# Performance work log

Hardware: AMD Instinct MI355X
Metric: run time of the kernel (lower is better)

The kernel has to match this reference:

```python
import jax, jax.numpy as jnp
import numpy as np

E, H = 1024, 16
N, S, T = 2, 2048, 2048


def setup_inputs() -> dict:
    key = jax.random.key(0)
    ks = jax.random.split(key, 8)
    scale = 1.0 / np.sqrt(E)
    q = jax.random.normal(ks[0], (N, S, E), dtype=jnp.float32)
    k = jax.random.normal(ks[1], (N, T, E), dtype=jnp.float32)
    v = jax.random.normal(ks[2], (N, T, E), dtype=jnp.float32)
    pad_mask = jax.random.randint(ks[3], (N, 1, 1, T), 0, 2, dtype=jnp.int32)
    subsq_mask = jnp.tril(jnp.ones((S, T), dtype=jnp.int32))[None, None]
    Wq = jax.random.normal(ks[4], (E, E), dtype=jnp.float32) * scale
    Wk = jax.random.normal(ks[5], (E, E), dtype=jnp.float32) * scale
    Wv = jax.random.normal(ks[6], (E, E), dtype=jnp.float32) * scale
    bq = jnp.zeros((E,), dtype=jnp.float32)
    bk = jnp.zeros((E,), dtype=jnp.float32)
    bv = jnp.zeros((E,), dtype=jnp.float32)
    return {"query": q, "key": k, "value": v, "pad_mask": pad_mask,
            "subsq_mask": subsq_mask, "Wq": Wq, "bq": bq, "Wk": Wk,
            "bk": bk, "Wv": Wv, "bv": bv}


def reference(query, key, value, pad_mask, subsq_mask, Wq, bq, Wk, bk, Wv, bv):
    n, s, e = query.shape
    t = value.shape[1]
    d = e // H
    # Linear projections (torch Linear: x @ W^T + b), split into heads
    q = (query @ Wq.T + bq).reshape(n, s, H, d).transpose(0, 2, 1, 3)  # [N,H,S,D]
    k = (key @ Wk.T + bk).reshape(n, t, H, d).transpose(0, 2, 1, 3)    # [N,H,T,D]
    v = (value @ Wv.T + bv).reshape(n, t, H, d).transpose(0, 2, 1, 3)  # [N,H,T,D]
    att = jnp.einsum('bhsd,bhtd->bhst', q, k) / jnp.sqrt(jnp.float32(d))
    att = jnp.where(pad_mask == 0, jnp.float32(-1e9), att)
    att = jnp.where(subsq_mask == 0, jnp.float32(-1e9), att)
    prob = jax.nn.softmax(att, axis=-1)
    out = jnp.einsum('bhst,bhtd->bhsd', prob, v)  # [N,H,S,D]
    return out.transpose(0, 2, 1, 3).reshape(n, s, e)
```

## Files before the change

kernel.cpp:

```cpp
#include <hip/hip_runtime.h>

#define HEADS 16
#define DH    64
#define EMB   1024
#define NBAT  2
#define SEQ   2048
#define KDIM  1024
#define NROW  (NBAT * SEQ)

typedef __attribute__((ext_vector_type(8))) short short8;
typedef __attribute__((ext_vector_type(4))) short short4v;
typedef __attribute__((ext_vector_type(4))) float floatx4;
typedef unsigned short u16;
typedef unsigned int   u32;
typedef unsigned long long u64;

__device__ __forceinline__ u16 f2bf(float x) {
    u32 u = __builtin_bit_cast(u32, x);
    u += 0x7fffu + ((u >> 16) & 1u);
    return (u16)(u >> 16);
}
__device__ __forceinline__ float bf2f(u16 v) {
    return __builtin_bit_cast(float, ((u32)v) << 16);
}

__device__ __forceinline__ void gll16(const u16* g, u16* l) {
    __builtin_amdgcn_global_load_lds((const __attribute__((address_space(1))) u32*)g,
                                     (__attribute__((address_space(3))) u32*)l, 16, 0, 0);
}

__global__ __launch_bounds__(256) void cvt_kernel(
    const float* __restrict__ q, const float* __restrict__ k, const float* __restrict__ v,
    const float* __restrict__ wq, const float* __restrict__ wk, const float* __restrict__ wv,
    u16* __restrict__ xb, u16* __restrict__ wb)
{
    const int z = blockIdx.y;
    const float* src; u16* dst; int n;
    if (z < 3) { src = (z == 0) ? q : (z == 1) ? k : v;     dst = xb + (size_t)z * 4194304;       n = 4194304; }
    else       { src = (z == 3) ? wq : (z == 4) ? wk : wv;  dst = wb + (size_t)(z - 3) * 1048576; n = 1048576; }
    for (int i = (blockIdx.x * 256 + threadIdx.x) * 8; i < n; i += 512 * 256 * 8) {
        float4 a = *(const float4*)(src + i);
        float4 b = *(const float4*)(src + i + 4);
        short8 o;
        o[0] = (short)f2bf(a.x); o[1] = (short)f2bf(a.y); o[2] = (short)f2bf(a.z); o[3] = (short)f2bf(a.w);
        o[4] = (short)f2bf(b.x); o[5] = (short)f2bf(b.y); o[6] = (short)f2bf(b.z); o[7] = (short)f2bf(b.w);
        *(short8*)(dst + i) = o;
    }
}

__global__ __launch_bounds__(256) void proj_kernel(
    const u16* __restrict__ xb, const u16* __restrict__ wb,
    const float* __restrict__ bq, const float* __restrict__ bk, const float* __restrict__ bv,
    u16* __restrict__ qh, u16* __restrict__ kh, u16* __restrict__ vt)
{
    const int f = blockIdx.x;
    const int xcd = f & 7, jj = f >> 3;
    const int g  = xcd * 12 + (jj >> 3);
    const int nx = jj & 7;
    const int z  = g >> 5, y = g & 31;

    const u16* A  = xb + (size_t)z * 4194304;
    const u16* B  = wb + (size_t)z * 1048576;
    const float* Bp = (z == 0) ? bq : (z == 1) ? bk : bv;
    u16* dst        = (z == 0) ? qh : (z == 1) ? kh : vt;

    const int m0 = y * 128;
    const int n0 = nx * 128;
    const int tid  = threadIdx.x;
    const int wave = tid >> 6, lane = tid & 63;
    const int quad = lane >> 4, l15 = lane & 15;
    const int waveM = wave >> 1, waveN = wave & 1;
    const int sw = l15 & 7;

    __shared__ __align__(16) u16 smem[2 * 128 * 64];
    u16* As = smem;
    u16* Bs = smem + 128 * 64;

    floatx4 acc[4][4];
    for (int a = 0; a < 4; a++)
        for (int b = 0; b < 4; b++)
            acc[a][b] = floatx4{0.f, 0.f, 0.f, 0.f};

    const int lrow = lane >> 3;
    const int gcol = ((lane & 7) ^ lrow) * 8;

    for (int k0 = 0; k0 < KDIM; k0 += 64) {
        for (int j = 0; j < 4; j++) {
            int r8 = wave * 32 + j * 8;
            gll16(A + (size_t)(m0 + r8 + lrow) * KDIM + k0 + gcol, &As[r8 * 64]);
        }
        for (int j = 0; j < 4; j++) {
            int r8 = wave * 32 + j * 8;
            gll16(B + (size_t)(n0 + r8 + lrow) * KDIM + k0 + gcol, &Bs[r8 * 64]);
        }
        __syncthreads();

        for (int ks = 0; ks < 2; ks++) {
            short8 af[4], bfg[4];
            for (int mb = 0; mb < 4; mb++)
                af[mb]  = *(const short8*)&As[(waveM * 64 + mb * 16 + l15) * 64 + ((ks * 4 + quad) ^ sw) * 8];
            for (int nb = 0; nb < 4; nb++)
                bfg[nb] = *(const short8*)&Bs[(waveN * 64 + nb * 16 + l15) * 64 + ((ks * 4 + quad) ^ sw) * 8];
            for (int mb = 0; mb < 4; mb++)
                for (int nb = 0; nb < 4; nb++)
                    acc[mb][nb] = __builtin_amdgcn_mfma_f32_16x16x32_bf16(af[mb], bfg[nb], acc[mb][nb], 0, 0, 0);
        }
        __syncthreads();
    }

    if (z != 2) {
        const int row0 = m0 + waveM * 64;
        const int col0 = n0 + waveN * 64;
        const float scale = (z == 0) ? 0.125f * 1.44269504f : 1.0f;
        for (int nb = 0; nb < 4; nb++) {
            int col = col0 + nb * 16 + l15;
            float bias = Bp[col];
            int hh = col >> 6, dd = col & 63;
            for (int mb = 0; mb < 4; mb++) {
                for (int r = 0; r < 4; r++) {
                    int row = row0 + mb * 16 + quad * 4 + r;
                    int nn = row >> 11, ss = row & 2047;
                    dst[((size_t)(nn * HEADS + hh) * SEQ + ss) * DH + dd] =
                        f2bf((acc[mb][nb][r] + bias) * scale);
                }
            }
        }
    } else {
        const int nn  = m0 >> 11;
        const int ss0 = m0 & 2047;
        for (int p = 0; p < 2; p++) {
            if (waveN == p) {
                for (int nb = 0; nb < 4; nb++) {
                    int col_l = nb * 16 + l15;
                    float bias = Bp[n0 + p * 64 + col_l];
                    for (int mb = 0; mb < 4; mb++) {
                        short4v pk;
                        for (int r = 0; r < 4; r++)
                            pk[r] = (short)f2bf(acc[mb][nb][r] + bias);
                        *(short4v*)&smem[col_l * 136 + waveM * 64 + mb * 16 + quad * 4] = pk;
                    }
                }
            }
            __syncthreads();
            const int hh = (n0 >> 6) + p;
            u16* drow = dst + ((size_t)(nn * HEADS + hh) * DH) * SEQ + ss0;
            for (int c2 = tid; c2 < 1024; c2 += 256) {
                int dl = c2 >> 4, tc = (c2 & 15) * 8;
                short8 vv = *(const short8*)&smem[dl * 136 + tc];
                *(short8*)(drow + (size_t)dl * SEQ + tc) = vv;
            }
            __syncthreads();
        }
    }
}

__global__ __launch_bounds__(256) void vmean_kernel(const u16* __restrict__ vt,
                                                    float* __restrict__ vmean)
{
    const int row = blockIdx.x;
    const u16* p = vt + (size_t)row * SEQ;
    const int tid = threadIdx.x;
    float s = 0.f;
    for (int i = tid; i < SEQ; i += 256) s += bf2f(p[i]);
    __shared__ float red[256];
    red[tid] = s;
    __syncthreads();
    for (int st = 128; st > 0; st >>= 1) {
        if (tid < st) red[tid] += red[tid + st];
        __syncthreads();
    }
    if (tid == 0) vmean[row] = red[0] * (1.f / (float)SEQ);
}

__global__ __launch_bounds__(256) void attn_kernel(
    const u16* __restrict__ qh, const u16* __restrict__ kh, const u16* __restrict__ vt,
    const int* __restrict__ pad, const float* __restrict__ vmean,
    float* __restrict__ out)
{
    const int f = blockIdx.x;
    const int xcd = f & 7, jj = f >> 3;
    const int nh = xcd * 4 + (jj >> 4);
    const int pr = jj & 15;
    const int n = nh >> 4, h = nh & 15;
    const int tid  = threadIdx.x;
    const int wave = tid >> 6, lane = tid & 63;
    const int quad = lane >> 4, l15 = lane & 15;
    const int sw = l15 & 7;

    __shared__ __align__(16) u16 Ks[2][64 * 64];
    __shared__ __align__(16) u16 Vs[2][64 * 64];
    __shared__ __align__(16) u16 Ps[64 * 72];
    __shared__ u64 padb[32];

    {
        const int* pp = pad + n * SEQ;
        for (int i = 0; i < 8; i++) {
            int seg = wave * 8 + i;
            u64 m = __ballot(pp[seg * 64 + lane] != 0);
            if (lane == 0) padb[seg] = m;
        }
    }

    const u16* qbase = qh + (size_t)nh * SEQ * DH;
    const u16* kbase = kh + (size_t)nh * SEQ * DH;
    const u16* vbase = vt + (size_t)nh * DH * SEQ;

    short8 ones;
    for (int i = 0; i < 8; i++) ones[i] = (short)0x3F80;
    float vm[4];
    for (int nd = 0; nd < 4; nd++) vm[nd] = vmean[nh * DH + nd * 16 + l15];

    const int lrow = lane >> 3;
    const int gcol = ((lane & 7) ^ lrow) * 8;

    for (int half = 0; half < 2; half++) {
        const int sb = half ? (31 - pr) : pr;
        const int s0 = sb * 64;
        const int nt = sb + 1;
        const int srow = s0 + wave * 16 + l15;

        short8 qf[2];
        for (int ks = 0; ks < 2; ks++)
            qf[ks] = *(const short8*)(qbase + (size_t)srow * DH + ks * 32 + quad * 8);

        floatx4 oacc[4], lacc;
        for (int nd = 0; nd < 4; nd++) oacc[nd] = floatx4{0.f, 0.f, 0.f, 0.f};
        lacc = floatx4{0.f, 0.f, 0.f, 0.f};

        __syncthreads();

        for (int j = 0; j < 2; j++) {
            int r8 = wave * 16 + j * 8;
            gll16(kbase + (size_t)(r8 + lrow) * DH + gcol, &Ks[0][r8 * 64]);
            gll16(vbase + (size_t)(r8 + lrow) * SEQ + gcol, &Vs[0][r8 * 64]);
        }

        for (int tb = 0; tb < nt; tb++) {
            const int cur = tb & 1;
            __syncthreads();

            if (tb + 1 < nt) {
                const int t0n = (tb + 1) * 64;
                for (int j = 0; j < 2; j++) {
                    int r8 = wave * 16 + j * 8;
                    gll16(kbase + (size_t)(t0n + r8 + lrow) * DH + gcol, &Ks[1 - cur][r8 * 64]);
                    gll16(vbase + (size_t)(r8 + lrow) * SEQ + t0n + gcol, &Vs[1 - cur][r8 * 64]);
                }
            }

            const int t0 = tb * 64;
            const u64 w = padb[t0 >> 6];
            const bool diag = (tb == sb);

            floatx4 sc[4];
            for (int nb = 0; nb < 4; nb++) sc[nb] = floatx4{0.f, 0.f, 0.f, 0.f};
            for (int ks = 0; ks < 2; ks++)
                for (int nb = 0; nb < 4; nb++) {
                    short8 kf = *(const short8*)&Ks[cur][(nb * 16 + l15) * 64 + ((ks * 4 + quad) ^ sw) * 8];
                    sc[nb] = __builtin_amdgcn_mfma_f32_16x16x32_bf16(kf, qf[ks], sc[nb], 0, 0, 0);
                }

            for (int nb = 0; nb < 4; nb++) {
                short4v pk;
                for (int r = 0; r < 4; r++) {
                    int sh = nb * 16 + quad * 4 + r;
                    bool ok = ((w >> sh) & 1ull) != 0;
                    if (diag) ok = ok && (t0 + sh <= srow);
                    float p = ok ? __builtin_amdgcn_exp2f(sc[nb][r]) : 0.f;
                    pk[r] = (short)f2bf(p);
                }
                *(short4v*)&Ps[(wave * 16 + l15) * 72 + nb * 16 + quad * 4] = pk;
            }
            asm volatile("s_waitcnt lgkmcnt(0)" ::: "memory");

            for (int ks = 0; ks < 2; ks++) {
                short8 pa = *(const short8*)&Ps[(wave * 16 + l15) * 72 + ks * 32 + quad * 8];
                for (int nd = 0; nd < 4; nd++) {
                    short8 vb = *(const short8*)&Vs[cur][(nd * 16 + l15) * 64 + ((ks * 4 + quad) ^ sw) * 8];
                    oacc[nd] = __builtin_amdgcn_mfma_f32_16x16x32_bf16(pa, vb, oacc[nd], 0, 0, 0);
                }
                lacc = __builtin_amdgcn_mfma_f32_16x16x32_bf16(pa, ones, lacc, 0, 0, 0);
            }
        }

        for (int r = 0; r < 4; r++) {
            float l = lacc[r];
            int s = s0 + wave * 16 + quad * 4 + r;
            float* orow = out + (size_t)(n * SEQ + s) * EMB + h * DH;
            if (l > 0.f) {
                float inv = 1.f / l;
                for (int nd = 0; nd < 4; nd++) orow[nd * 16 + l15] = oacc[nd][r] * inv;
            } else {
                for (int nd = 0; nd < 4; nd++) orow[nd * 16 + l15] = vm[nd];
            }
        }
    }
}

extern "C" void kernel_launch(void* const* d_in, const int* in_sizes, int n_in,
                              void* d_out, int out_size, void* d_ws, size_t ws_size,
                              hipStream_t stream)
{
    const float* qin = (const float*)d_in[0];
    const float* kin = (const float*)d_in[1];
    const float* vin = (const float*)d_in[2];
    const int*   pad = (const int*)d_in[3];
    const float* Wq = (const float*)d_in[5];
    const float* bq = (const float*)d_in[6];
    const float* Wk = (const float*)d_in[7];
    const float* bk = (const float*)d_in[8];
    const float* Wv = (const float*)d_in[9];
    const float* bv = (const float*)d_in[10];
    float* out = (float*)d_out;

    const size_t per = (size_t)NBAT * HEADS * SEQ * DH;
    u16* qh = (u16*)d_ws;
    u16* kh = qh + per;
    u16* vt = kh + per;
    float* vmean = (float*)(vt + per);
    u16* xb = (u16*)(vmean + 2048);
    u16* wb = xb + 3 * per;

    cvt_kernel<<<dim3(512, 6), 256, 0, stream>>>(qin, kin, vin, Wq, Wk, Wv, xb, wb);
    proj_kernel<<<dim3(768), 256, 0, stream>>>(xb, wb, bq, bk, bv, qh, kh, vt);
    vmean_kernel<<<dim3(NBAT * HEADS * DH), 256, 0, stream>>>(vt, vmean);
    attn_kernel<<<dim3(512), 256, 0, stream>>>(qh, kh, vt, pad, vmean, out);
}
```

Measured before the change: 216.4 us.

## Split attention key range across two blocks and merge partial outputs

The attention grid is doubled so that each (head, query-pair) is handled by two blocks, each processing alternate 64-key tiles. Unnormalized partial outputs and row sums go to a workspace that reuses the bf16 scratch, and a new merge kernel sums them and applies normalization or the fully-masked fallback. V is now single-buffered with an extra barrier, and bf16 packing switches to truncation via a permute. The aim is more parallelism and occupancy, paid for with extra fp32 partial-result traffic, one more launch, and slightly different rounding.

```diff
diff --git a/kernel.cpp b/kernel.cpp
--- a/kernel.cpp
+++ b/kernel.cpp
@@ -22,6 +22,10 @@
 }
 __device__ __forceinline__ float bf2f(u16 v) {
     return __builtin_bit_cast(float, ((u32)v) << 16);
+}
+__device__ __forceinline__ u32 pack_bf16_trunc(float lo, float hi) {
+    return __builtin_amdgcn_perm(__builtin_bit_cast(u32, hi),
+                                 __builtin_bit_cast(u32, lo), 0x07060302u);
 }
 
 __device__ __forceinline__ void gll16(const u16* g, u16* l) {
@@ -172,23 +176,23 @@
     if (tid == 0) vmean[row] = red[0] * (1.f / (float)SEQ);
 }
 
-__global__ __launch_bounds__(256) void attn_kernel(
+__global__ __launch_bounds__(256, 4) void attn_kernel(
     const u16* __restrict__ qh, const u16* __restrict__ kh, const u16* __restrict__ vt,
-    const int* __restrict__ pad, const float* __restrict__ vmean,
-    float* __restrict__ out)
+    const int* __restrict__ pad, float* __restrict__ po, float* __restrict__ pl)
 {
     const int f = blockIdx.x;
     const int xcd = f & 7, jj = f >> 3;
-    const int nh = xcd * 4 + (jj >> 4);
-    const int pr = jj & 15;
-    const int n = nh >> 4, h = nh & 15;
+    const int nh = xcd * 4 + (jj >> 5);
+    const int rem = jj & 31;
+    const int pr = rem >> 1, sp = rem & 1;
+    const int n = nh >> 4;
     const int tid  = threadIdx.x;
     const int wave = tid >> 6, lane = tid & 63;
     const int quad = lane >> 4, l15 = lane & 15;
     const int sw = l15 & 7;
 
     __shared__ __align__(16) u16 Ks[2][64 * 64];
-    __shared__ __align__(16) u16 Vs[2][64 * 64];
+    __shared__ __align__(16) u16 Vs[64 * 64];
     __shared__ __align__(16) u16 Ps[64 * 72];
     __shared__ u64 padb[32];
 
@@ -207,16 +211,17 @@
 
     short8 ones;
     for (int i = 0; i < 8; i++) ones[i] = (short)0x3F80;
-    float vm[4];
-    for (int nd = 0; nd < 4; nd++) vm[nd] = vmean[nh * DH + nd * 16 + l15];
 
     const int lrow = lane >> 3;
     const int gcol = ((lane & 7) ^ lrow) * 8;
+
+    float* pobase = po + (size_t)(sp * 2 * HEADS + nh) * SEQ * DH;
+    float* plbase = pl + (size_t)(sp * 2 * HEADS + nh) * SEQ;
 
     for (int half = 0; half < 2; half++) {
         const int sb = half ? (31 - pr) : pr;
         const int s0 = sb * 64;
-        const int nt = sb + 1;
+        const int count = (sb >= sp) ? ((sb - sp) >> 1) + 1 : 0;
         const int srow = s0 + wave * 16 + l15;
 
         short8 qf[2];
@@ -229,27 +234,31 @@
 
         __syncthreads();
 
-        for (int j = 0; j < 2; j++) {
-            int r8 = wave * 16 + j * 8;
-            gll16(kbase + (size_t)(r8 + lrow) * DH + gcol, &Ks[0][r8 * 64]);
-            gll16(vbase + (size_t)(r8 + lrow) * SEQ + gcol, &Vs[0][r8 * 64]);
-        }
-
-        for (int tb = 0; tb < nt; tb++) {
-            const int cur = tb & 1;
+        if (count > 0) {
+            for (int j = 0; j < 2; j++) {
+                int r8 = wave * 16 + j * 8;
+                gll16(kbase + (size_t)(sp * 64 + r8 + lrow) * DH + gcol, &Ks[0][r8 * 64]);
+            }
+        }
+
+        for (int i = 0; i < count; i++) {
+            const int tb = sp + 2 * i;
+            const int t0 = tb * 64;
+            const int cur = i & 1;
             __syncthreads();
 
-            if (tb + 1 < nt) {
-                const int t0n = (tb + 1) * 64;
+            for (int j = 0; j < 2; j++) {
+                int r8 = wave * 16 + j * 8;
+                gll16(vbase + (size_t)(r8 + lrow) * SEQ + t0 + gcol, &Vs[r8 * 64]);
+            }
+            if (i + 1 < count) {
                 for (int j = 0; j < 2; j++) {
                     int r8 = wave * 16 + j * 8;
-                    gll16(kbase + (size_t)(t0n + r8 + lrow) * DH + gcol, &Ks[1 - cur][r8 * 64]);
-                    gll16(vbase + (size_t)(r8 + lrow) * SEQ + t0n + gcol, &Vs[1 - cur][r8 * 64]);
-                }
-            }
-
-            const int t0 = tb * 64;
-            const u64 w = padb[t0 >> 6];
+                    gll16(kbase + (size_t)(t0 + 128 + r8 + lrow) * DH + gcol, &Ks[1 - cur][r8 * 64]);
+                }
+            }
+
+            const u64 w = padb[tb];
             const bool diag = (tb == sb);
 
             floatx4 sc[4];
@@ -261,22 +270,25 @@
                 }
 
             for (int nb = 0; nb < 4; nb++) {
-                short4v pk;
+                float p[4];
                 for (int r = 0; r < 4; r++) {
                     int sh = nb * 16 + quad * 4 + r;
                     bool ok = ((w >> sh) & 1ull) != 0;
                     if (diag) ok = ok && (t0 + sh <= srow);
-                    float p = ok ? __builtin_amdgcn_exp2f(sc[nb][r]) : 0.f;
-                    pk[r] = (short)f2bf(p);
-                }
-                *(short4v*)&Ps[(wave * 16 + l15) * 72 + nb * 16 + quad * 4] = pk;
+                    p[r] = ok ? __builtin_amdgcn_exp2f(sc[nb][r]) : 0.f;
+                }
+                uint2 pk;
+                pk.x = pack_bf16_trunc(p[0], p[1]);
+                pk.y = pack_bf16_trunc(p[2], p[3]);
+                *(uint2*)&Ps[(wave * 16 + l15) * 72 + nb * 16 + quad * 4] = pk;
             }
             asm volatile("s_waitcnt lgkmcnt(0)" ::: "memory");
+            __syncthreads();
 
             for (int ks = 0; ks < 2; ks++) {
                 short8 pa = *(const short8*)&Ps[(wave * 16 + l15) * 72 + ks * 32 + quad * 8];
                 for (int nd = 0; nd < 4; nd++) {
-                    short8 vb = *(const short8*)&Vs[cur][(nd * 16 + l15) * 64 + ((ks * 4 + quad) ^ sw) * 8];
+                    short8 vb = *(const short8*)&Vs[(nd * 16 + l15) * 64 + ((ks * 4 + quad) ^ sw) * 8];
                     oacc[nd] = __builtin_amdgcn_mfma_f32_16x16x32_bf16(pa, vb, oacc[nd], 0, 0, 0);
                 }
                 lacc = __builtin_amdgcn_mfma_f32_16x16x32_bf16(pa, ones, lacc, 0, 0, 0);
@@ -284,17 +296,39 @@
         }
 
         for (int r = 0; r < 4; r++) {
-            float l = lacc[r];
             int s = s0 + wave * 16 + quad * 4 + r;
-            float* orow = out + (size_t)(n * SEQ + s) * EMB + h * DH;
-            if (l > 0.f) {
-                float inv = 1.f / l;
-                for (int nd = 0; nd < 4; nd++) orow[nd * 16 + l15] = oacc[nd][r] * inv;
-            } else {
-                for (int nd = 0; nd < 4; nd++) orow[nd * 16 + l15] = vm[nd];
-            }
-        }
-    }
+            float* orow = pobase + (size_t)s * DH;
+            for (int nd = 0; nd < 4; nd++) orow[nd * 16 + l15] = oacc[nd][r];
+            if (l15 == 0) plbase[s] = lacc[r];
+        }
+    }
+}
+
+__global__ __launch_bounds__(256) void merge_kernel(
+    const float* __restrict__ po, const float* __restrict__ pl,
+    const float* __restrict__ vmean, float* __restrict__ out)
+{
+    const int ns = blockIdx.x;
+    const int n = ns >> 11, s = ns & 2047;
+    const int c = threadIdx.x;
+    const int h = c >> 4, d4 = (c & 15) * 4;
+    const int nh = n * HEADS + h;
+    const size_t PSTRIDE  = (size_t)2 * HEADS * SEQ * DH;
+    const size_t LSTRIDE  = (size_t)2 * HEADS * SEQ;
+    const size_t idx = ((size_t)nh * SEQ + s) * DH + d4;
+
+    float4 a = *(const float4*)(po + idx);
+    float4 b = *(const float4*)(po + PSTRIDE + idx);
+    float l = pl[(size_t)nh * SEQ + s] + pl[LSTRIDE + (size_t)nh * SEQ + s];
+    float4 o;
+    if (l > 0.f) {
+        float inv = 1.f / l;
+        o.x = (a.x + b.x) * inv; o.y = (a.y + b.y) * inv;
+        o.z = (a.z + b.z) * inv; o.w = (a.w + b.w) * inv;
+    } else {
+        o = *(const float4*)(vmean + nh * DH + d4);
+    }
+    *(float4*)(out + ((size_t)(n * SEQ + s)) * EMB + c * 4) = o;
 }
 
 extern "C" void kernel_launch(void* const* d_in, const int* in_sizes, int n_in,
@@ -318,11 +352,16 @@
     u16* kh = qh + per;
     u16* vt = kh + per;
     float* vmean = (float*)(vt + per);
-    u16* xb = (u16*)(vmean + 2048);
+    char* scratch = (char*)(vmean + 2048);
+    u16* xb = (u16*)scratch;
     u16* wb = xb + 3 * per;
+    float* po = (float*)scratch;
+    float* pl = po + (size_t)2 * HEADS * NBAT * SEQ * DH / 1 * 1;
+    pl = po + (size_t)2 * 2 * HEADS * SEQ * DH;
 
     cvt_kernel<<<dim3(512, 6), 256, 0, stream>>>(qin, kin, vin, Wq, Wk, Wv, xb, wb);
     proj_kernel<<<dim3(768), 256, 0, stream>>>(xb, wb, bq, bk, bv, qh, kh, vt);
     vmean_kernel<<<dim3(NBAT * HEADS * DH), 256, 0, stream>>>(vt, vmean);
-    attn_kernel<<<dim3(512), 256, 0, stream>>>(qh, kh, vt, pad, vmean, out);
-}
+    attn_kernel<<<dim3(1024), 256, 0, stream>>>(qh, kh, vt, pad, po, pl);
+    merge_kernel<<<dim3(NBAT * SEQ), 256, 0, stream>>>(po, pl, vmean, out);
+}
```

Result: slower. 228.2 us (+5.5%).

## Split attention KV loop across two wave groups and merge partial outputs

Applied to the files above, without the earlier changes.

The attention block grows to 512 threads in two 4-wave groups. Each group handles alternating KV tiles for the same query tile, keeping its own K/V/P buffers, and the partial output and row sums are combined through shared memory at the end. This aims to shorten the serial KV loop per block and raise the number of waves in flight. P is also packed to bf16 by truncation with a perm instruction instead of round-to-nearest. The cost is extra barriers, uneven tile counts between the two groups, a cross-group reduction, and slightly lower rounding precision for P.

```diff
diff --git a/kernel.cpp b/kernel.cpp
--- a/kernel.cpp
+++ b/kernel.cpp
@@ -22,6 +22,10 @@
 }
 __device__ __forceinline__ float bf2f(u16 v) {
     return __builtin_bit_cast(float, ((u32)v) << 16);
+}
+__device__ __forceinline__ u32 pack_bf16_trunc(float lo, float hi) {
+    return __builtin_amdgcn_perm(__builtin_bit_cast(u32, hi),
+                                 __builtin_bit_cast(u32, lo), 0x07060302u);
 }
 
 __device__ __forceinline__ void gll16(const u16* g, u16* l) {
@@ -172,7 +176,7 @@
     if (tid == 0) vmean[row] = red[0] * (1.f / (float)SEQ);
 }
 
-__global__ __launch_bounds__(256) void attn_kernel(
+__global__ __launch_bounds__(512, 4) void attn_kernel(
     const u16* __restrict__ qh, const u16* __restrict__ kh, const u16* __restrict__ vt,
     const int* __restrict__ pad, const float* __restrict__ vmean,
     float* __restrict__ out)
@@ -183,19 +187,22 @@
     const int pr = jj & 15;
     const int n = nh >> 4, h = nh & 15;
     const int tid  = threadIdx.x;
-    const int wave = tid >> 6, lane = tid & 63;
+    const int wave = tid >> 6;
+    const int grp  = wave >> 2;
+    const int w4   = wave & 3;
+    const int lane = tid & 63;
     const int quad = lane >> 4, l15 = lane & 15;
     const int sw = l15 & 7;
 
-    __shared__ __align__(16) u16 Ks[2][64 * 64];
+    __shared__ __align__(16) u16 Ks[2][2][64 * 64];
     __shared__ __align__(16) u16 Vs[2][64 * 64];
-    __shared__ __align__(16) u16 Ps[64 * 72];
+    __shared__ __align__(16) u16 Ps[2][64 * 72];
     __shared__ u64 padb[32];
 
     {
         const int* pp = pad + n * SEQ;
-        for (int i = 0; i < 8; i++) {
-            int seg = wave * 8 + i;
+        for (int i = 0; i < 4; i++) {
+            int seg = wave * 4 + i;
             u64 m = __ballot(pp[seg * 64 + lane] != 0);
             if (lane == 0) padb[seg] = m;
         }
@@ -212,86 +219,117 @@
 
     const int lrow = lane >> 3;
     const int gcol = ((lane & 7) ^ lrow) * 8;
+    const floatx4 zero4 = floatx4{0.f, 0.f, 0.f, 0.f};
+
+    float* odump = (float*)&Ks[1][0][0];
+    float* ldump = (float*)&Ps[1][0];
 
     for (int half = 0; half < 2; half++) {
         const int sb = half ? (31 - pr) : pr;
         const int s0 = sb * 64;
-        const int nt = sb + 1;
-        const int srow = s0 + wave * 16 + l15;
+        const int cnt  = (sb >= grp) ? ((sb - grp) >> 1) + 1 : 0;
+        const int maxc = (sb >> 1) + 1;
+        const int srow = s0 + w4 * 16 + l15;
 
         short8 qf[2];
         for (int ks = 0; ks < 2; ks++)
             qf[ks] = *(const short8*)(qbase + (size_t)srow * DH + ks * 32 + quad * 8);
 
         floatx4 oacc[4], lacc;
-        for (int nd = 0; nd < 4; nd++) oacc[nd] = floatx4{0.f, 0.f, 0.f, 0.f};
-        lacc = floatx4{0.f, 0.f, 0.f, 0.f};
-
-        __syncthreads();
-
-        for (int j = 0; j < 2; j++) {
-            int r8 = wave * 16 + j * 8;
-            gll16(kbase + (size_t)(r8 + lrow) * DH + gcol, &Ks[0][r8 * 64]);
-            gll16(vbase + (size_t)(r8 + lrow) * SEQ + gcol, &Vs[0][r8 * 64]);
-        }
-
-        for (int tb = 0; tb < nt; tb++) {
-            const int cur = tb & 1;
+        for (int nd = 0; nd < 4; nd++) oacc[nd] = zero4;
+        lacc = zero4;
+
+        __syncthreads();
+
+        if (cnt > 0) {
+            for (int j = 0; j < 2; j++) {
+                int r8 = w4 * 16 + j * 8;
+                gll16(kbase + (size_t)(grp * 64 + r8 + lrow) * DH + gcol, &Ks[grp][0][r8 * 64]);
+            }
+        }
+
+        for (int i = 0; i < maxc; i++) {
+            const bool act = (i < cnt);
+            const int tb = grp + 2 * i;
+            const int t0 = tb * 64;
+            const int cur = i & 1;
             __syncthreads();
 
-            if (tb + 1 < nt) {
-                const int t0n = (tb + 1) * 64;
+            if (act) {
                 for (int j = 0; j < 2; j++) {
-                    int r8 = wave * 16 + j * 8;
-                    gll16(kbase + (size_t)(t0n + r8 + lrow) * DH + gcol, &Ks[1 - cur][r8 * 64]);
-                    gll16(vbase + (size_t)(r8 + lrow) * SEQ + t0n + gcol, &Vs[1 - cur][r8 * 64]);
-                }
-            }
-
-            const int t0 = tb * 64;
-            const u64 w = padb[t0 >> 6];
-            const bool diag = (tb == sb);
-
-            floatx4 sc[4];
-            for (int nb = 0; nb < 4; nb++) sc[nb] = floatx4{0.f, 0.f, 0.f, 0.f};
-            for (int ks = 0; ks < 2; ks++)
+                    int r8 = w4 * 16 + j * 8;
+                    gll16(vbase + (size_t)(r8 + lrow) * SEQ + t0 + gcol, &Vs[grp][r8 * 64]);
+                }
+                if (i + 1 < cnt) {
+                    for (int j = 0; j < 2; j++) {
+                        int r8 = w4 * 16 + j * 8;
+                        gll16(kbase + (size_t)(t0 + 128 + r8 + lrow) * DH + gcol, &Ks[grp][1 - cur][r8 * 64]);
+                    }
+                }
+
+                const u64 w = padb[tb];
+                const bool diag = (tb == sb);
+
+                floatx4 sc[4];
+                for (int nb = 0; nb < 4; nb++) sc[nb] = zero4;
+                for (int ks = 0; ks < 2; ks++)
+                    for (int nb = 0; nb < 4; nb++) {
+                        short8 kf = *(const short8*)&Ks[grp][cur][(nb * 16 + l15) * 64 + ((ks * 4 + quad) ^ sw) * 8];
+                        sc[nb] = __builtin_amdgcn_mfma_f32_16x16x32_bf16(kf, qf[ks], sc[nb], 0, 0, 0);
+                    }
+
                 for (int nb = 0; nb < 4; nb++) {
-                    short8 kf = *(const short8*)&Ks[cur][(nb * 16 + l15) * 64 + ((ks * 4 + quad) ^ sw) * 8];
-                    sc[nb] = __builtin_amdgcn_mfma_f32_16x16x32_bf16(kf, qf[ks], sc[nb], 0, 0, 0);
-                }
-
-            for (int nb = 0; nb < 4; nb++) {
-                short4v pk;
-                for (int r = 0; r < 4; r++) {
-                    int sh = nb * 16 + quad * 4 + r;
-                    bool ok = ((w >> sh) & 1ull) != 0;
-                    if (diag) ok = ok && (t0 + sh <= srow);
-                    float p = ok ? __builtin_amdgcn_exp2f(sc[nb][r]) : 0.f;
-                    pk[r] = (short)f2bf(p);
-                }
-                *(short4v*)&Ps[(wave * 16 + l15) * 72 + nb * 16 + quad * 4] = pk;
-            }
-            asm volatile("s_waitcnt lgkmcnt(0)" ::: "memory");
-
-            for (int ks = 0; ks < 2; ks++) {
-                short8 pa = *(const short8*)&Ps[(wave * 16 + l15) * 72 + ks * 32 + quad * 8];
-                for (int nd = 0; nd < 4; nd++) {
-                    short8 vb = *(const short8*)&Vs[cur][(nd * 16 + l15) * 64 + ((ks * 4 + quad) ^ sw) * 8];
-                    oacc[nd] = __builtin_amdgcn_mfma_f32_16x16x32_bf16(pa, vb, oacc[nd], 0, 0, 0);
-                }
-                lacc = __builtin_amdgcn_mfma_f32_16x16x32_bf16(pa, ones, lacc, 0, 0, 0);
-            }
-        }
-
-        for (int r = 0; r < 4; r++) {
-            float l = lacc[r];
-            int s = s0 + wave * 16 + quad * 4 + r;
-            float* orow = out + (size_t)(n * SEQ + s) * EMB + h * DH;
-            if (l > 0.f) {
-                float inv = 1.f / l;
-                for (int nd = 0; nd < 4; nd++) orow[nd * 16 + l15] = oacc[nd][r] * inv;
-            } else {
-                for (int nd = 0; nd < 4; nd++) orow[nd * 16 + l15] = vm[nd];
+                    float p[4];
+                    for (int r = 0; r < 4; r++) {
+                        int sh = nb * 16 + quad * 4 + r;
+                        bool ok = ((w >> sh) & 1ull) != 0;
+                        if (diag) ok = ok && (t0 + sh <= srow);
+                        p[r] = ok ? __builtin_amdgcn_exp2f(sc[nb][r]) : 0.f;
+                    }
+                    uint2 pk;
+                    pk.x = pack_bf16_trunc(p[0], p[1]);
+                    pk.y = pack_bf16_trunc(p[2], p[3]);
+                    *(uint2*)&Ps[grp][(w4 * 16 + l15) * 72 + nb * 16 + quad * 4] = pk;
+                }
+                asm volatile("s_waitcnt lgkmcnt(0)" ::: "memory");
+            }
+            __syncthreads();
+
+            if (act) {
+                for (int ks = 0; ks < 2; ks++) {
+                    short8 pa = *(const short8*)&Ps[grp][(w4 * 16 + l15) * 72 + ks * 32 + quad * 8];
+                    for (int nd = 0; nd < 4; nd++) {
+                        short8 vb = *(const short8*)&Vs[grp][(nd * 16 + l15) * 64 + ((ks * 4 + quad) ^ sw) * 8];
+                        oacc[nd] = __builtin_amdgcn_mfma_f32_16x16x32_bf16(pa, vb, oacc[nd], 0, 0, 0);
+                    }
+                    lacc = __builtin_amdgcn_mfma_f32_16x16x32_bf16(pa, ones, lacc, 0, 0, 0);
+                }
+            }
+        }
+
+        __syncthreads();
+        if (grp == 1) {
+            for (int r = 0; r < 4; r++) {
+                int sl = w4 * 16 + quad * 4 + r;
+                for (int nd = 0; nd < 4; nd++)
+                    odump[sl * 64 + nd * 16 + l15] = oacc[nd][r];
+                if (l15 == 0) ldump[sl] = lacc[r];
+            }
+        }
+        __syncthreads();
+        if (grp == 0) {
+            for (int r = 0; r < 4; r++) {
+                int sl = w4 * 16 + quad * 4 + r;
+                int s = s0 + sl;
+                float l = lacc[r] + ldump[sl];
+                float* orow = out + (size_t)(n * SEQ + s) * EMB + h * DH;
+                if (l > 0.f) {
+                    float inv = 1.f / l;
+                    for (int nd = 0; nd < 4; nd++)
+                        orow[nd * 16 + l15] = (oacc[nd][r] + odump[sl * 64 + nd * 16 + l15]) * inv;
+                } else {
+                    for (int nd = 0; nd < 4; nd++) orow[nd * 16 + l15] = vm[nd];
+                }
             }
         }
     }
@@ -324,5 +362,5 @@
     cvt_kernel<<<dim3(512, 6), 256, 0, stream>>>(qin, kin, vin, Wq, Wk, Wv, xb, wb);
     proj_kernel<<<dim3(768), 256, 0, stream>>>(xb, wb, bq, bk, bv, qh, kh, vt);
     vmean_kernel<<<dim3(NBAT * HEADS * DH), 256, 0, stream>>>(vt, vmean);
-    attn_kernel<<<dim3(512), 256, 0, stream>>>(qh, kh, vt, pad, vmean, out);
-}
+    attn_kernel<<<dim3(512), 512, 0, stream>>>(qh, kh, vt, pad, vmean, out);
+}
```

Result: slower. 226.0 us (+4.4%).
